# Kernel optimization log

Measured on AMD Instinct MI355X. Metric: run time of the kernel, lower is better.

The kernel has to match this reference:

```python
import jax, jax.numpy as jnp
import numpy as np

BN_EPS = 1e-5

def setup_inputs() -> dict:
    key = jax.random.key(0)
    ks = jax.random.split(key, 8)
    B, Cin, H, W = 4, 256, 64, 64
    Cqk, Cout = 128, 256
    x = jax.random.normal(ks[0], (B, Cin, H, W), dtype=jnp.float32)
    # 1x1 convs == per-pixel linear maps: weight [out, in], bias [out]
    Wq = jax.random.normal(ks[1], (Cqk, Cin), dtype=jnp.float32) * 0.05
    bq = jax.random.normal(ks[2], (Cqk,), dtype=jnp.float32) * 0.05
    Wk = jax.random.normal(ks[3], (Cqk, Cin), dtype=jnp.float32) * 0.05
    bk = jax.random.normal(ks[4], (Cqk,), dtype=jnp.float32) * 0.05
    Wv = jax.random.normal(ks[5], (Cout, Cin), dtype=jnp.float32) * 0.05
    bv = jax.random.normal(ks[6], (Cout,), dtype=jnp.float32) * 0.05
    gamma = jnp.ones((Cout,), dtype=jnp.float32)
    beta = jnp.zeros((Cout,), dtype=jnp.float32)
    return {"x": x, "Wq": Wq, "bq": bq, "Wk": Wk, "bk": bk,
            "Wv": Wv, "bv": bv, "gamma": gamma, "beta": beta}

def reference(x, Wq, bq, Wk, bk, Wv, bv, gamma, beta):
    B, Cin, H, W = x.shape
    N = H * W
    # 1x1 convs (per-pixel linear projections)
    q = jnp.einsum('bchw,oc->bohw', x, Wq) + bq[None, :, None, None]  # [B,Cqk,H,W]
    k = jnp.einsum('bchw,oc->bohw', x, Wk) + bk[None, :, None, None]  # [B,Cqk,H,W]
    v = jnp.einsum('bchw,oc->bohw', x, Wv) + bv[None, :, None, None]  # [B,Cout,H,W]
    # num_levels=1: bilinear interpolate to the same size is identity.
    qf = q.reshape(B, -1, N)   # [B,Cqk,N]
    kf = k.reshape(B, -1, N)   # [B,Cqk,N]
    vf = v.reshape(B, -1, N)   # [B,Cout,N]
    # score = q^T k, softmax over keys (no 1/sqrt(d) scaling, as in source)
    score = jnp.einsum('bcn,bcm->bnm', qf, kf)        # [B,N,N]
    att = jax.nn.softmax(score, axis=2)               # [B,N,N]
    w = jnp.einsum('bnm,bcm->bcn', att, vf)           # [B,Cout,N]
    merged = w.reshape(B, -1, H, W)                   # [B,Cout,H,W]
    # BatchNorm2d in training mode: batch stats over (B,H,W), biased variance
    mean = jnp.mean(merged, axis=(0, 2, 3), keepdims=True)
    var = jnp.var(merged, axis=(0, 2, 3), keepdims=True)
    norm = (merged - mean) * jax.lax.rsqrt(var + BN_EPS)
    return norm * gamma[None, :, None, None] + beta[None, :, None, None]
```

## Files before the change

kernel.cpp:

```cpp
#include <hip/hip_runtime.h>
#include <hip/hip_bf16.h>

typedef __attribute__((ext_vector_type(8))) _Float16 hfrag;
typedef __attribute__((ext_vector_type(4))) float ffrag;
typedef __attribute__((ext_vector_type(8))) unsigned short us8;
typedef __attribute__((ext_vector_type(4))) unsigned short us4;

#define DEVINL static __device__ __forceinline__
#define MFMAH(a, b, c)  __builtin_amdgcn_mfma_f32_16x16x32_f16((a), (b), (c), 0, 0, 0)

DEVINL void gload_lds16(const _Float16* g, _Float16* l) {
    __builtin_amdgcn_global_load_lds(
        (const __attribute__((address_space(1))) unsigned int*)g,
        (__attribute__((address_space(3))) unsigned int*)l, 16, 0, 0);
}

DEVINL int pkh(float a, float b) {
    typedef __attribute__((ext_vector_type(2))) __fp16 fp16x2;
    fp16x2 t = __builtin_amdgcn_cvt_pkrtz(a, b);
    union { fp16x2 h; int i; } u; u.h = t; return u.i;
}

DEVINL int permV(int p) {
    return (p & 35) | ((p & 8) << 1) | ((p & 4) << 1) | ((p & 16) >> 2);
}

__global__ void kprep(const float* __restrict__ Wq, const float* __restrict__ Wk,
                      const float* __restrict__ Wv, const float* __restrict__ bq,
                      const float* __restrict__ bk, const float* __restrict__ bv,
                      _Float16* __restrict__ Wh, float* __restrict__ ball) {
    int t = blockIdx.x * 256 + threadIdx.x;
    int o = t >> 8, c = t & 255;
    float v = (o < 128) ? Wq[o * 256 + c]
            : (o < 256) ? Wk[(o - 128) * 256 + c]
                        : Wv[(o - 256) * 256 + c];
    Wh[t] = (_Float16)v;
    if (c == 0) {
        ball[o] = (o < 128) ? bq[o] : (o < 256) ? bk[o - 128] : bv[o - 256];
    }
}

__global__ __launch_bounds__(256) void kproj(const float* __restrict__ x,
                                             const _Float16* __restrict__ Wh,
                                             const float* __restrict__ ball,
                                             _Float16* __restrict__ Qb,
                                             _Float16* __restrict__ Kb,
                                             _Float16* __restrict__ Vb) {
    __shared__ _Float16 sX[64 * 256];
    const int t = threadIdx.x;
    const int lane = t & 63;
    const int wv = t >> 6;
    const int l16 = lane & 15;
    const int lg = lane >> 4;
    const int b = blockIdx.x >> 6;
    const int n0 = (blockIdx.x & 63) << 6;
    const float* xb = x + (size_t)b * 256 * 4096 + n0;

    const int p = lane;
#pragma unroll
    for (int ci = 0; ci < 8; ++ci) {
        const int c0 = ci * 32 + (wv << 3);
        __align__(16) _Float16 th[8];
#pragma unroll
        for (int j = 0; j < 8; ++j) th[j] = (_Float16)xb[(size_t)(c0 + j) * 4096 + p];
        *(us8*)&sX[p * 256 + (c0 ^ ((p & 7) << 3))] = *(const us8*)th;
    }
    __syncthreads();

    ffrag accQK[16];
    ffrag accV[16];
#pragma unroll
    for (int i = 0; i < 16; ++i) {
        accQK[i] = ffrag{0.f, 0.f, 0.f, 0.f};
        accV[i]  = ffrag{0.f, 0.f, 0.f, 0.f};
    }
    const int rowx = 16 * wv + l16;
#pragma unroll
    for (int step = 0; step < 8; ++step) {
        const int cb = step * 32 + (lg << 3);
        hfrag ax = *(const hfrag*)&sX[rowx * 256 + (cb ^ ((rowx & 7) << 3))];
#pragma unroll
        for (int ct = 0; ct < 16; ++ct) {
            const int o = ct * 16 + l16;
            hfrag bw = *(const hfrag*)&Wh[o * 256 + cb];
            accQK[ct] = MFMAH(ax, bw, accQK[ct]);
        }
        hfrag bx[4];
#pragma unroll
        for (int c2 = 0; c2 < 4; ++c2) {
            const int px = c2 * 16 + l16;
            bx[c2] = *(const hfrag*)&sX[px * 256 + (cb ^ ((px & 7) << 3))];
        }
#pragma unroll
        for (int mt = 0; mt < 4; ++mt) {
            const int o = 256 + 64 * wv + 16 * mt + l16;
            hfrag aw = *(const hfrag*)&Wh[o * 256 + cb];
#pragma unroll
            for (int c2 = 0; c2 < 4; ++c2)
                accV[mt * 4 + c2] = MFMAH(aw, bx[c2], accV[mt * 4 + c2]);
        }
    }

#pragma unroll
    for (int ct = 0; ct < 16; ++ct) {
        const int o = ct * 16 + l16;
        const float bias = ball[o];
        _Float16* dst = (o < 128) ? Qb : Kb;
        const int oo = o & 127;
#pragma unroll
        for (int r = 0; r < 4; ++r) {
            const int px = 16 * wv + (lg << 2) + r;
            dst[((size_t)b * 4096 + n0 + px) * 128 + oo] = (_Float16)(accQK[ct][r] + bias);
        }
    }
#pragma unroll
    for (int mt = 0; mt < 4; ++mt) {
#pragma unroll
        for (int r = 0; r < 4; ++r) {
            const int o = 64 * wv + 16 * mt + (lg << 2) + r;
            const float bias = ball[256 + o];
#pragma unroll
            for (int c2 = 0; c2 < 4; ++c2) {
                const int px = c2 * 16 + l16;
                Vb[((size_t)b * 256 + o) * 4096 + n0 + permV(px)] =
                    (_Float16)(accV[mt * 4 + c2][r] + bias);
            }
        }
    }
}

__global__ __launch_bounds__(512, 2) void kattn(const _Float16* __restrict__ Qb,
                                                const _Float16* __restrict__ Kb,
                                                const _Float16* __restrict__ Vb,
                                                _Float16* __restrict__ pO,
                                                float* __restrict__ pML) {
    __shared__ __align__(16) _Float16 smem[49664];
    float* sml = (float*)(smem + 49152);

    const int t = threadIdx.x;
    const int lane = t & 63;
    const int wv = t >> 6;
    const int qg = wv & 3;
    const int kh = wv >> 2;
    const int l16 = lane & 15;
    const int lg = lane >> 4;

    const int blk = blockIdx.x;
    const int x8 = blk & 7;
    const int b = x8 >> 1;
    const int ksel = x8 & 1;
    const int qt5 = blk >> 3;
    const int n0 = qt5 << 7;
    const int kb = ksel << 11;

    const _Float16* Kg = Kb + (size_t)b * 4096 * 128;
    const _Float16* Vg = Vb + (size_t)b * 256 * 4096;

    hfrag aq0[4], aq1[4];
    {
        const size_t gq0 = ((size_t)b * 4096 + n0 + qg * 32 + l16) * 128;
        const size_t gq1 = gq0 + 16 * 128;
#pragma unroll
        for (int st = 0; st < 4; ++st) {
            aq0[st] = *(const hfrag*)&Qb[gq0 + st * 32 + lg * 8];
            aq1[st] = *(const hfrag*)&Qb[gq1 + st * 32 + lg * 8];
        }
    }

    float m0 = -3e38f, l0 = 0.f;
    float m1 = -3e38f, l1 = 0.f;
    ffrag O0[16], O1[16];
#pragma unroll
    for (int i = 0; i < 16; ++i) {
        O0[i] = ffrag{0.f, 0.f, 0.f, 0.f};
        O1[i] = ffrag{0.f, 0.f, 0.f, 0.f};
    }
    hfrag pb0p, pb1p;

    const int krow_in = lane >> 4;
    const int kcol = lane & 15;
    const int vrow_in = lane >> 3;
    const int vcol = lane & 7;

    auto STAGEK = [&](int it, int bsel) {
        const int k0 = kb + (it << 6);
        _Float16* sK = smem + (bsel << 13);
#pragma unroll
        for (int j = 0; j < 2; ++j) {
            const int c = 2 * wv + j;
            const int row = 4 * c + krow_in;
            gload_lds16(Kg + (size_t)(k0 + row) * 128 + ((kcol ^ (row & 7)) << 3),
                        sK + c * 512);
        }
    };
    auto STAGEV = [&](int it, int bsel) {
        const int k0 = kb + (it << 6);
        _Float16* sV = smem + 16384 + (bsel << 14);
#pragma unroll
        for (int j = 0; j < 4; ++j) {
            const int cv = 4 * wv + j;
            const int co = 8 * cv + vrow_in;
            gload_lds16(Vg + (size_t)co * 4096 + k0 + ((vcol ^ (co & 7)) << 3),
                        sV + cv * 512);
        }
    };

    auto PV = [&](int bsel) {
        const _Float16* sV = smem + 16384 + (bsel << 14);
#pragma unroll
        for (int ct = 0; ct < 16; ++ct) {
            const int co = ct * 16 + l16;
            hfrag av = *(const hfrag*)&sV[co * 64 + ((kh * 32 + lg * 8) ^ ((co & 7) << 3))];
            O0[ct] = MFMAH(av, pb0p, O0[ct]);
            O1[ct] = MFMAH(av, pb1p, O1[ct]);
        }
    };

    STAGEK(0, 0);
    STAGEV(0, 0);
    __builtin_amdgcn_sched_barrier(0);

#pragma unroll 1
    for (int it = 0; it < 32; ++it) {
        asm volatile("s_waitcnt vmcnt(4)" ::: "memory");
        __builtin_amdgcn_s_barrier();
        __builtin_amdgcn_sched_barrier(0);
        STAGEK((it + 1) & 31, (it + 1) & 1);
        __builtin_amdgcn_sched_barrier(0);

        const _Float16* sK = smem + ((it & 1) << 13);

        __builtin_amdgcn_s_setprio(1);
        ffrag S00 = ffrag{0.f,0.f,0.f,0.f}, S01 = ffrag{0.f,0.f,0.f,0.f};
        ffrag S10 = ffrag{0.f,0.f,0.f,0.f}, S11 = ffrag{0.f,0.f,0.f,0.f};
#pragma unroll
        for (int kt = 0; kt < 2; ++kt) {
            const int rowk = kh * 32 + kt * 16 + l16;
            const int swz = (rowk & 7) << 3;
#pragma unroll
            for (int st = 0; st < 4; ++st) {
                hfrag ak = *(const hfrag*)&sK[rowk * 128 + ((st * 32 + lg * 8) ^ swz)];
                if (kt == 0) {
                    S00 = MFMAH(ak, aq0[st], S00);
                    S10 = MFMAH(ak, aq1[st], S10);
                } else {
                    S01 = MFMAH(ak, aq0[st], S01);
                    S11 = MFMAH(ak, aq1[st], S11);
                }
            }
        }
        if (it > 0) PV((it - 1) & 1);
        __builtin_amdgcn_s_setprio(0);

        float mx0 = fmaxf(fmaxf(fmaxf(S00[0], S00[1]), fmaxf(S00[2], S00[3])),
                          fmaxf(fmaxf(S01[0], S01[1]), fmaxf(S01[2], S01[3])));
        float mx1 = fmaxf(fmaxf(fmaxf(S10[0], S10[1]), fmaxf(S10[2], S10[3])),
                          fmaxf(fmaxf(S11[0], S11[1]), fmaxf(S11[2], S11[3])));
        mx0 = fmaxf(mx0, __shfl_xor(mx0, 16));
        mx0 = fmaxf(mx0, __shfl_xor(mx0, 32));
        mx1 = fmaxf(mx1, __shfl_xor(mx1, 16));
        mx1 = fmaxf(mx1, __shfl_xor(mx1, 32));
        if (__any((mx0 > m0 + 8.f) || (mx1 > m1 + 8.f))) {
            const float nm0 = fmaxf(m0, mx0), nm1 = fmaxf(m1, mx1);
            const float sc0 = __expf(m0 - nm0), sc1 = __expf(m1 - nm1);
            m0 = nm0; m1 = nm1;
            l0 *= sc0; l1 *= sc1;
#pragma unroll
            for (int i = 0; i < 16; ++i) {
#pragma unroll
                for (int r = 0; r < 4; ++r) {
                    O0[i][r] *= sc0;
                    O1[i][r] *= sc1;
                }
            }
        }
        float e00[4], e01[4], e10[4], e11[4];
        float rs0 = 0.f, rs1 = 0.f;
#pragma unroll
        for (int r = 0; r < 4; ++r) {
            e00[r] = __expf(S00[r] - m0);
            e01[r] = __expf(S01[r] - m0);
            e10[r] = __expf(S10[r] - m1);
            e11[r] = __expf(S11[r] - m1);
            rs0 += e00[r] + e01[r];
            rs1 += e10[r] + e11[r];
        }
        rs0 += __shfl_xor(rs0, 16);
        rs0 += __shfl_xor(rs0, 32);
        rs1 += __shfl_xor(rs1, 16);
        rs1 += __shfl_xor(rs1, 32);
        l0 += rs0;
        l1 += rs1;

        {
            union { int i[4]; hfrag h; } u;
            u.i[0] = pkh(e00[0], e00[1]);
            u.i[1] = pkh(e00[2], e00[3]);
            u.i[2] = pkh(e01[0], e01[1]);
            u.i[3] = pkh(e01[2], e01[3]);
            pb0p = u.h;
            u.i[0] = pkh(e10[0], e10[1]);
            u.i[1] = pkh(e10[2], e10[3]);
            u.i[2] = pkh(e11[0], e11[1]);
            u.i[3] = pkh(e11[2], e11[3]);
            pb1p = u.h;
        }

        __builtin_amdgcn_s_barrier();
        __builtin_amdgcn_sched_barrier(0);
        STAGEV((it + 1) & 31, (it + 1) & 1);
        __builtin_amdgcn_sched_barrier(0);
    }

    asm volatile("s_waitcnt vmcnt(0)" ::: "memory");
    __builtin_amdgcn_s_barrier();
    PV(1);

    __syncthreads();
    _Float16* sE = smem;
    const int r0 = qg * 32 + l16;
    const int r1 = r0 + 16;
    const int rsw0 = (r0 & 7) << 3;
    const int rsw1 = (r1 & 7) << 3;
    if (kh == 1) {
        const float inv0 = 1.f / l0, inv1 = 1.f / l1;
#pragma unroll
        for (int ct = 0; ct < 16; ++ct)
#pragma unroll
            for (int r = 0; r < 4; ++r) {
                const int col = ct * 16 + lg * 4 + r;
                sE[r0 * 256 + (col ^ rsw0)] = (_Float16)(O0[ct][r] * inv0);
                sE[r1 * 256 + (col ^ rsw1)] = (_Float16)(O1[ct][r] * inv1);
            }
        if (lg == 0) {
            ((float2*)sml)[r0] = make_float2(m0, l0);
            ((float2*)sml)[r1] = make_float2(m1, l1);
        }
    }
    __syncthreads();
    const size_t mlbase = (size_t)(ksel * 4 + b) * 4096 + n0;
    if (kh == 0) {
        const float2 pml0 = ((const float2*)sml)[r0];
        const float2 pml1 = ((const float2*)sml)[r1];
        const float M0 = fmaxf(m0, pml0.x), M1 = fmaxf(m1, pml1.x);
        const float a0 = __expf(m0 - M0), c0 = __expf(pml0.x - M0);
        const float a1 = __expf(m1 - M1), c1 = __expf(pml1.x - M1);
        const float nl0 = a0 * l0 + c0 * pml0.y;
        const float nl1 = a1 * l1 + c1 * pml1.y;
        const float wa0 = a0 / nl0, wb0 = c0 * pml0.y / nl0;
        const float wa1 = a1 / nl1, wb1 = c1 * pml1.y / nl1;
        if (lg == 0) {
            ((float2*)pML)[mlbase + r0] = make_float2(M0, nl0);
            ((float2*)pML)[mlbase + r1] = make_float2(M1, nl1);
        }
#pragma unroll
        for (int ct = 0; ct < 16; ++ct)
#pragma unroll
            for (int r = 0; r < 4; ++r) {
                const int col = ct * 16 + lg * 4 + r;
                const int i0 = r0 * 256 + (col ^ rsw0);
                const int i1 = r1 * 256 + (col ^ rsw1);
                const float v0 = (float)sE[i0];
                const float v1 = (float)sE[i1];
                sE[i0] = (_Float16)(wa0 * O0[ct][r] + wb0 * v0);
                sE[i1] = (_Float16)(wa1 * O1[ct][r] + wb1 * v1);
            }
    }
    __syncthreads();
    const size_t obase = ((size_t)(ksel * 4 + b) * 4096 + n0) * 256;
#pragma unroll
    for (int i = 0; i < 8; ++i) {
        const int idx = i * 512 + t;
        const int px = idx >> 5;
        const int cg = idx & 31;
        *(us8*)&pO[obase + (size_t)px * 256 + cg * 8] =
            *(const us8*)&sE[px * 256 + (cg ^ (px & 7)) * 8];
    }
}

__global__ __launch_bounds__(256) void kmerge(const _Float16* __restrict__ pO,
                                              const float* __restrict__ pML,
                                              _Float16* __restrict__ wbuf,
                                              float* __restrict__ part) {
    __shared__ float sacc[2048];
    __shared__ float sacc2[2048];
    const int t = threadIdx.x;
    const int rowloc = t >> 5;
    const int co8 = (t & 31) * 8;
    float s[8], s2[8];
#pragma unroll
    for (int j = 0; j < 8; ++j) { s[j] = 0.f; s2[j] = 0.f; }
#pragma unroll 2
    for (int i = 0; i < 8; ++i) {
        const int g = blockIdx.x * 64 + i * 8 + rowloc;
        const float2 ml0 = ((const float2*)pML)[g];
        const float2 ml1 = ((const float2*)pML)[16384 + g];
        const float M = fmaxf(ml0.x, ml1.x);
        const float a = __expf(ml0.x - M) * ml0.y;
        const float c = __expf(ml1.x - M) * ml1.y;
        const float inv = 1.f / (a + c);
        const float wa = a * inv, wc = c * inv;
        hfrag o0 = *(const hfrag*)&pO[(size_t)g * 256 + co8];
        hfrag o1 = *(const hfrag*)&pO[(size_t)(16384 + g) * 256 + co8];
        hfrag w;
#pragma unroll
        for (int j = 0; j < 8; ++j) {
            const float v = wa * (float)o0[j] + wc * (float)o1[j];
            w[j] = (_Float16)v;
            s[j] += v;
            s2[j] += v * v;
        }
        *(hfrag*)&wbuf[(size_t)g * 256 + co8] = w;
    }
#pragma unroll
    for (int j = 0; j < 8; ++j) {
        sacc[rowloc * 256 + co8 + j] = s[j];
        sacc2[rowloc * 256 + co8 + j] = s2[j];
    }
    __syncthreads();
    float p = 0.f, p2 = 0.f;
#pragma unroll
    for (int rl = 0; rl < 8; ++rl) {
        p  += sacc[rl * 256 + t];
        p2 += sacc2[rl * 256 + t];
    }
    part[blockIdx.x * 512 + t] = p;
    part[blockIdx.x * 512 + 256 + t] = p2;
}

__global__ void kstats2(const float* __restrict__ partial, float* __restrict__ stats) {
    const int ch = blockIdx.x;
    const int j = threadIdx.x;
    float s = 0.f;
#pragma unroll
    for (int i = 0; i < 4; ++i)
        s += partial[(size_t)(j + 64 * i) * 512 + ch];
    s += __shfl_xor(s, 1);
    s += __shfl_xor(s, 2);
    s += __shfl_xor(s, 4);
    s += __shfl_xor(s, 8);
    s += __shfl_xor(s, 16);
    s += __shfl_xor(s, 32);
    if (j == 0) stats[ch] = s;
}

__global__ __launch_bounds__(256) void kapply(const _Float16* __restrict__ w,
                                              const float* __restrict__ stats,
                                              const float* __restrict__ gamma,
                                              const float* __restrict__ beta,
                                              float* __restrict__ out) {
    __shared__ _Float16 sw[64 * 260];
    __shared__ float sscale[256];
    __shared__ float sshift[256];
    const int t = threadIdx.x;
    const int b = blockIdx.x >> 6;
    const int n0 = (blockIdx.x & 63) << 6;
    const _Float16* wb = w + ((size_t)b * 4096 + n0) * 256;
#pragma unroll
    for (int i = 0; i < 16; ++i) {
        const int chunk = i * 256 + t;
        const int p = chunk >> 6;
        const int cq = chunk & 63;
        *(us4*)&sw[p * 260 + cq * 4] = *(const us4*)&wb[p * 256 + cq * 4];
    }
    {
        const float mean = stats[t] * (1.f / 16384.f);
        const float var = stats[256 + t] * (1.f / 16384.f) - mean * mean;
        const float inv = rsqrtf(var + 1e-5f);
        const float sc = gamma[t] * inv;
        sscale[t] = sc;
        sshift[t] = beta[t] - mean * sc;
    }
    __syncthreads();
    const int p = t & 63;
    const int cg = t >> 6;
    float* ob = out + (size_t)b * 256 * 4096 + n0;
#pragma unroll 4
    for (int i = 0; i < 64; ++i) {
        const int co = i * 4 + cg;
        const float v = (float)sw[p * 260 + co];
        ob[(size_t)co * 4096 + p] = v * sscale[co] + sshift[co];
    }
}

extern "C" void kernel_launch(void* const* d_in, const int* in_sizes, int n_in,
                              void* d_out, int out_size, void* d_ws, size_t ws_size,
                              hipStream_t stream) {
    const float* x     = (const float*)d_in[0];
    const float* Wq    = (const float*)d_in[1];
    const float* bq    = (const float*)d_in[2];
    const float* Wk    = (const float*)d_in[3];
    const float* bk    = (const float*)d_in[4];
    const float* Wv    = (const float*)d_in[5];
    const float* bv    = (const float*)d_in[6];
    const float* gamma = (const float*)d_in[7];
    const float* beta  = (const float*)d_in[8];
    float* out = (float*)d_out;

    char* ws = (char*)d_ws;
    _Float16* Wh    = (_Float16*)(ws + 0x0);
    float*    pML   = (float*)(ws + 0x0);
    float*    ball  = (float*)(ws + 0x40000);
    float*    stats = (float*)(ws + 0x40800);
    float*    part  = (float*)(ws + 0x41000);
    _Float16* Qb    = (_Float16*)(ws + 0x100000);
    _Float16* Kb    = (_Float16*)(ws + 0x500000);
    _Float16* wbuf  = (_Float16*)(ws + 0x100000);
    _Float16* Vb    = (_Float16*)(ws + 0x900000);
    _Float16* pO    = (_Float16*)(ws + 0x1100000);
    if (ws_size < 0x2100000) return;

    kprep<<<512, 256, 0, stream>>>(Wq, Wk, Wv, bq, bk, bv, Wh, ball);
    kproj<<<256, 256, 0, stream>>>(x, Wh, ball, Qb, Kb, Vb);
    kattn<<<256, 512, 0, stream>>>(Qb, Kb, Vb, pO, pML);
    kmerge<<<256, 256, 0, stream>>>(pO, pML, wbuf, part);
    kstats2<<<512, 64, 0, stream>>>(part, stats);
    kapply<<<256, 256, 0, stream>>>(wbuf, stats, gamma, beta, out);
}
```

Baseline: 134.8 us.

## Fuse merge, stats and BN apply into one cooperative kernel with grid sync

Replaces the kmerge, kstats2 and kapply kernels with a single cooperative kernel. Each block keeps its merged fp16 tile in shared memory, writes partial sums, and uses a grid sync before reducing stats and another before applying the normalization. This drops two kernel launches and the global round-trip of the merged buffer. In exchange it adds two grid-wide barriers and requires all 256 blocks to be co-resident.

```diff
diff --git a/kernel.cpp b/kernel.cpp
--- a/kernel.cpp
+++ b/kernel.cpp
@@ -1,5 +1,6 @@
 #include <hip/hip_runtime.h>
 #include <hip/hip_bf16.h>
+#include <hip/hip_cooperative_groups.h>
 
 typedef __attribute__((ext_vector_type(8))) _Float16 hfrag;
 typedef __attribute__((ext_vector_type(4))) float ffrag;
@@ -378,21 +379,29 @@
     }
 }
 
-__global__ __launch_bounds__(256) void kmerge(const _Float16* __restrict__ pO,
-                                              const float* __restrict__ pML,
-                                              _Float16* __restrict__ wbuf,
-                                              float* __restrict__ part) {
-    __shared__ float sacc[2048];
-    __shared__ float sacc2[2048];
+__global__ __launch_bounds__(256) void ktail(const _Float16* __restrict__ pO,
+                                             const float* __restrict__ pML,
+                                             const float* __restrict__ gamma,
+                                             const float* __restrict__ beta,
+                                             float* __restrict__ part,
+                                             float* __restrict__ stats,
+                                             float* __restrict__ out) {
+    __shared__ __align__(16) unsigned char sm[50176];
+    _Float16* sw = (_Float16*)sm;
+    float* sacc  = (float*)(sm + 33792);
+    float* sacc2 = sacc + 2048;
+
     const int t = threadIdx.x;
+    const int bid = blockIdx.x;
     const int rowloc = t >> 5;
     const int co8 = (t & 31) * 8;
+
     float s[8], s2[8];
 #pragma unroll
     for (int j = 0; j < 8; ++j) { s[j] = 0.f; s2[j] = 0.f; }
 #pragma unroll 2
     for (int i = 0; i < 8; ++i) {
-        const int g = blockIdx.x * 64 + i * 8 + rowloc;
+        const int g = bid * 64 + i * 8 + rowloc;
         const float2 ml0 = ((const float2*)pML)[g];
         const float2 ml1 = ((const float2*)pML)[16384 + g];
         const float M = fmaxf(ml0.x, ml1.x);
@@ -410,7 +419,7 @@
             s[j] += v;
             s2[j] += v * v;
         }
-        *(hfrag*)&wbuf[(size_t)g * 256 + co8] = w;
+        *(hfrag*)&sw[(i * 8 + rowloc) * 264 + co8] = w;
     }
 #pragma unroll
     for (int j = 0; j < 8; ++j) {
@@ -424,45 +433,31 @@
         p  += sacc[rl * 256 + t];
         p2 += sacc2[rl * 256 + t];
     }
-    part[blockIdx.x * 512 + t] = p;
-    part[blockIdx.x * 512 + 256 + t] = p2;
-}
-
-__global__ void kstats2(const float* __restrict__ partial, float* __restrict__ stats) {
-    const int ch = blockIdx.x;
-    const int j = threadIdx.x;
-    float s = 0.f;
-#pragma unroll
-    for (int i = 0; i < 4; ++i)
-        s += partial[(size_t)(j + 64 * i) * 512 + ch];
-    s += __shfl_xor(s, 1);
-    s += __shfl_xor(s, 2);
-    s += __shfl_xor(s, 4);
-    s += __shfl_xor(s, 8);
-    s += __shfl_xor(s, 16);
-    s += __shfl_xor(s, 32);
-    if (j == 0) stats[ch] = s;
-}
-
-__global__ __launch_bounds__(256) void kapply(const _Float16* __restrict__ w,
-                                              const float* __restrict__ stats,
-                                              const float* __restrict__ gamma,
-                                              const float* __restrict__ beta,
-                                              float* __restrict__ out) {
-    __shared__ _Float16 sw[64 * 260];
-    __shared__ float sscale[256];
-    __shared__ float sshift[256];
-    const int t = threadIdx.x;
-    const int b = blockIdx.x >> 6;
-    const int n0 = (blockIdx.x & 63) << 6;
-    const _Float16* wb = w + ((size_t)b * 4096 + n0) * 256;
-#pragma unroll
-    for (int i = 0; i < 16; ++i) {
-        const int chunk = i * 256 + t;
-        const int p = chunk >> 6;
-        const int cq = chunk & 63;
-        *(us4*)&sw[p * 260 + cq * 4] = *(const us4*)&wb[p * 256 + cq * 4];
-    }
+    part[(size_t)bid * 512 + t] = p;
+    part[(size_t)bid * 512 + 256 + t] = p2;
+
+    cooperative_groups::this_grid().sync();
+
+    {
+        const int half = t >> 7;
+        const int j = t & 127;
+        const int ch = 2 * bid + half;
+        float v = part[(size_t)j * 512 + ch] + part[(size_t)(j + 128) * 512 + ch];
+        float* red = sacc;
+        red[t] = v;
+        __syncthreads();
+#pragma unroll
+        for (int off = 64; off >= 1; off >>= 1) {
+            if ((t & 127) < off) red[t] += red[t + off];
+            __syncthreads();
+        }
+        if ((t & 127) == 0) stats[ch] = red[t];
+    }
+
+    cooperative_groups::this_grid().sync();
+
+    float* sscale = sacc;
+    float* sshift = sacc + 256;
     {
         const float mean = stats[t] * (1.f / 16384.f);
         const float var = stats[256 + t] * (1.f / 16384.f) - mean * mean;
@@ -472,14 +467,16 @@
         sshift[t] = beta[t] - mean * sc;
     }
     __syncthreads();
-    const int p = t & 63;
-    const int cg = t >> 6;
+    const int px = t & 63;
+    const int cgp = t >> 6;
+    const int b = bid >> 6;
+    const int n0 = (bid & 63) << 6;
     float* ob = out + (size_t)b * 256 * 4096 + n0;
 #pragma unroll 4
     for (int i = 0; i < 64; ++i) {
-        const int co = i * 4 + cg;
-        const float v = (float)sw[p * 260 + co];
-        ob[(size_t)co * 4096 + p] = v * sscale[co] + sshift[co];
+        const int co = i * 4 + cgp;
+        const float v = (float)sw[px * 264 + co];
+        ob[(size_t)co * 4096 + px] = v * sscale[co] + sshift[co];
     }
 }
 
@@ -505,7 +502,6 @@
     float*    part  = (float*)(ws + 0x41000);
     _Float16* Qb    = (_Float16*)(ws + 0x100000);
     _Float16* Kb    = (_Float16*)(ws + 0x500000);
-    _Float16* wbuf  = (_Float16*)(ws + 0x100000);
     _Float16* Vb    = (_Float16*)(ws + 0x900000);
     _Float16* pO    = (_Float16*)(ws + 0x1100000);
     if (ws_size < 0x2100000) return;
@@ -513,7 +509,15 @@
     kprep<<<512, 256, 0, stream>>>(Wq, Wk, Wv, bq, bk, bv, Wh, ball);
     kproj<<<256, 256, 0, stream>>>(x, Wh, ball, Qb, Kb, Vb);
     kattn<<<256, 512, 0, stream>>>(Qb, Kb, Vb, pO, pML);
-    kmerge<<<256, 256, 0, stream>>>(pO, pML, wbuf, part);
-    kstats2<<<512, 64, 0, stream>>>(part, stats);
-    kapply<<<256, 256, 0, stream>>>(wbuf, stats, gamma, beta, out);
-}
+    {
+        const _Float16* a0 = pO;
+        const float* a1 = pML;
+        const float* a2 = gamma;
+        const float* a3 = beta;
+        float* a4 = part;
+        float* a5 = stats;
+        float* a6 = out;
+        void* args[] = {&a0, &a1, &a2, &a3, &a4, &a5, &a6};
+        hipLaunchCooperativeKernel((void*)ktail, dim3(256), dim3(256), args, 0, stream);
+    }
+}
```

Result: slower. 191.3 us (+41.9%).

## Fuse split-K merge and BN stats into attention via last-block atomic counter

Applied to the files above, without the earlier changes.

The separate merge and stats-reduction kernels are removed. Each attention block now writes its partial output and increments a per-tile counter. The second-arriving block of each pair reads its partner's partial from global memory and its own from LDS, combines them, writes the merged result into pO, and atomically accumulates the per-channel sum and sum-of-squares. This cuts two kernel launches and one full round trip of the own-half partial output through global memory, at the cost of an inter-block fence/atomic handshake and float atomics, which make the statistics order nondeterministic.

```diff
diff --git a/kernel.cpp b/kernel.cpp
--- a/kernel.cpp
+++ b/kernel.cpp
@@ -28,7 +28,8 @@
 __global__ void kprep(const float* __restrict__ Wq, const float* __restrict__ Wk,
                       const float* __restrict__ Wv, const float* __restrict__ bq,
                       const float* __restrict__ bk, const float* __restrict__ bv,
-                      _Float16* __restrict__ Wh, float* __restrict__ ball) {
+                      _Float16* __restrict__ Wh, float* __restrict__ ball,
+                      int* __restrict__ cnt, float* __restrict__ stats) {
     int t = blockIdx.x * 256 + threadIdx.x;
     int o = t >> 8, c = t & 255;
     float v = (o < 128) ? Wq[o * 256 + c]
@@ -37,6 +38,11 @@
     Wh[t] = (_Float16)v;
     if (c == 0) {
         ball[o] = (o < 128) ? bq[o] : (o < 256) ? bk[o - 128] : bv[o - 256];
+    }
+    if (blockIdx.x == 0 && threadIdx.x < 128) cnt[threadIdx.x] = 0;
+    if (blockIdx.x == 1) {
+        stats[threadIdx.x] = 0.f;
+        stats[256 + threadIdx.x] = 0.f;
     }
 }
 
@@ -133,9 +139,12 @@
                                                 const _Float16* __restrict__ Kb,
                                                 const _Float16* __restrict__ Vb,
                                                 _Float16* __restrict__ pO,
-                                                float* __restrict__ pML) {
-    __shared__ __align__(16) _Float16 smem[49664];
+                                                float* __restrict__ pML,
+                                                float* __restrict__ stats,
+                                                int* __restrict__ cnt) {
+    __shared__ __align__(16) _Float16 smem[50176];
     float* sml = (float*)(smem + 49152);
+    __shared__ int sWho;
 
     const int t = threadIdx.x;
     const int lane = t & 63;
@@ -372,76 +381,76 @@
     for (int i = 0; i < 8; ++i) {
         const int idx = i * 512 + t;
         const int px = idx >> 5;
-        const int cg = idx & 31;
-        *(us8*)&pO[obase + (size_t)px * 256 + cg * 8] =
-            *(const us8*)&sE[px * 256 + (cg ^ (px & 7)) * 8];
-    }
-}
-
-__global__ __launch_bounds__(256) void kmerge(const _Float16* __restrict__ pO,
-                                              const float* __restrict__ pML,
-                                              _Float16* __restrict__ wbuf,
-                                              float* __restrict__ part) {
-    __shared__ float sacc[2048];
-    __shared__ float sacc2[2048];
-    const int t = threadIdx.x;
-    const int rowloc = t >> 5;
-    const int co8 = (t & 31) * 8;
+        const int cg8 = idx & 31;
+        *(us8*)&pO[obase + (size_t)px * 256 + cg8 * 8] =
+            *(const us8*)&sE[px * 256 + (cg8 ^ (px & 7)) * 8];
+    }
+
+    __syncthreads();
+    if (t == 0) {
+        __threadfence();
+        sWho = atomicAdd(&cnt[blk >> 1], 1);
+    }
+    __syncthreads();
+    if (sWho == 0) return;
+    if (t == 0) __threadfence();
+    __syncthreads();
+
+    float* sWab = (float*)(smem + 49664);
+    const size_t mlbaseP = (size_t)((ksel ^ 1) * 4 + b) * 4096 + n0;
+    if (t < 128) {
+        const float2 mlP = ((const float2*)pML)[mlbaseP + t];
+        const float2 mlO = ((const float2*)pML)[mlbase + t];
+        const float M = fmaxf(mlP.x, mlO.x);
+        const float a = __expf(mlP.x - M) * mlP.y;
+        const float c = __expf(mlO.x - M) * mlO.y;
+        const float inv = 1.f / (a + c);
+        ((float2*)sWab)[t] = make_float2(a * inv, c * inv);
+    }
+    __syncthreads();
+
+    const size_t gbaseP = mlbaseP * 256;
+    const size_t gbase0 = ((size_t)b * 4096 + n0) * 256;
     float s[8], s2[8];
 #pragma unroll
     for (int j = 0; j < 8; ++j) { s[j] = 0.f; s2[j] = 0.f; }
+    const int cg8 = t & 31;
 #pragma unroll 2
     for (int i = 0; i < 8; ++i) {
-        const int g = blockIdx.x * 64 + i * 8 + rowloc;
-        const float2 ml0 = ((const float2*)pML)[g];
-        const float2 ml1 = ((const float2*)pML)[16384 + g];
-        const float M = fmaxf(ml0.x, ml1.x);
-        const float a = __expf(ml0.x - M) * ml0.y;
-        const float c = __expf(ml1.x - M) * ml1.y;
-        const float inv = 1.f / (a + c);
-        const float wa = a * inv, wc = c * inv;
-        hfrag o0 = *(const hfrag*)&pO[(size_t)g * 256 + co8];
-        hfrag o1 = *(const hfrag*)&pO[(size_t)(16384 + g) * 256 + co8];
+        const int px = i * 16 + (t >> 5);
+        const float2 wab = ((const float2*)sWab)[px];
+        hfrag po = *(const hfrag*)&pO[gbaseP + (size_t)px * 256 + cg8 * 8];
+        hfrag ow = *(const hfrag*)&sE[px * 256 + (cg8 ^ (px & 7)) * 8];
         hfrag w;
 #pragma unroll
         for (int j = 0; j < 8; ++j) {
-            const float v = wa * (float)o0[j] + wc * (float)o1[j];
+            const float v = wab.x * (float)po[j] + wab.y * (float)ow[j];
             w[j] = (_Float16)v;
             s[j] += v;
             s2[j] += v * v;
         }
-        *(hfrag*)&wbuf[(size_t)g * 256 + co8] = w;
-    }
+        *(hfrag*)&pO[gbase0 + (size_t)px * 256 + cg8 * 8] = w;
+    }
+
+    __syncthreads();
+    float* sacc  = (float*)smem;
+    float* sacc2 = sacc + 4096;
+    const int rg = t >> 5;
 #pragma unroll
     for (int j = 0; j < 8; ++j) {
-        sacc[rowloc * 256 + co8 + j] = s[j];
-        sacc2[rowloc * 256 + co8 + j] = s2[j];
-    }
-    __syncthreads();
-    float p = 0.f, p2 = 0.f;
-#pragma unroll
-    for (int rl = 0; rl < 8; ++rl) {
-        p  += sacc[rl * 256 + t];
-        p2 += sacc2[rl * 256 + t];
-    }
-    part[blockIdx.x * 512 + t] = p;
-    part[blockIdx.x * 512 + 256 + t] = p2;
-}
-
-__global__ void kstats2(const float* __restrict__ partial, float* __restrict__ stats) {
-    const int ch = blockIdx.x;
-    const int j = threadIdx.x;
-    float s = 0.f;
-#pragma unroll
-    for (int i = 0; i < 4; ++i)
-        s += partial[(size_t)(j + 64 * i) * 512 + ch];
-    s += __shfl_xor(s, 1);
-    s += __shfl_xor(s, 2);
-    s += __shfl_xor(s, 4);
-    s += __shfl_xor(s, 8);
-    s += __shfl_xor(s, 16);
-    s += __shfl_xor(s, 32);
-    if (j == 0) stats[ch] = s;
+        sacc [rg * 256 + cg8 * 8 + j] = s[j];
+        sacc2[rg * 256 + cg8 * 8 + j] = s2[j];
+    }
+    __syncthreads();
+    {
+        const int ch = t & 255;
+        const int sel = t >> 8;
+        const float* src = sel ? sacc2 : sacc;
+        float sum = 0.f;
+#pragma unroll
+        for (int rg2 = 0; rg2 < 16; ++rg2) sum += src[rg2 * 256 + ch];
+        atomicAdd(&stats[sel * 256 + ch], sum);
+    }
 }
 
 __global__ __launch_bounds__(256) void kapply(const _Float16* __restrict__ w,
@@ -502,18 +511,15 @@
     float*    pML   = (float*)(ws + 0x0);
     float*    ball  = (float*)(ws + 0x40000);
     float*    stats = (float*)(ws + 0x40800);
-    float*    part  = (float*)(ws + 0x41000);
+    int*      cnt   = (int*)(ws + 0x41000);
     _Float16* Qb    = (_Float16*)(ws + 0x100000);
     _Float16* Kb    = (_Float16*)(ws + 0x500000);
-    _Float16* wbuf  = (_Float16*)(ws + 0x100000);
     _Float16* Vb    = (_Float16*)(ws + 0x900000);
     _Float16* pO    = (_Float16*)(ws + 0x1100000);
     if (ws_size < 0x2100000) return;
 
-    kprep<<<512, 256, 0, stream>>>(Wq, Wk, Wv, bq, bk, bv, Wh, ball);
+    kprep<<<512, 256, 0, stream>>>(Wq, Wk, Wv, bq, bk, bv, Wh, ball, cnt, stats);
     kproj<<<256, 256, 0, stream>>>(x, Wh, ball, Qb, Kb, Vb);
-    kattn<<<256, 512, 0, stream>>>(Qb, Kb, Vb, pO, pML);
-    kmerge<<<256, 256, 0, stream>>>(pO, pML, wbuf, part);
-    kstats2<<<512, 64, 0, stream>>>(part, stats);
-    kapply<<<256, 256, 0, stream>>>(wbuf, stats, gamma, beta, out);
-}
+    kattn<<<256, 512, 0, stream>>>(Qb, Kb, Vb, pO, pML, stats, cnt);
+    kapply<<<256, 256, 0, stream>>>(pO, stats, gamma, beta, out);
+}
```

Measured after the change: 151.8 us. +12.6%, slower.

## Replace BN stats reduction kernel with atomics and double merge/apply grid size

Applied to the files above, without the earlier changes.

Drops the separate kstats2 launch. kmerge now atomically adds per-block channel sums and sums of squares into a global stats buffer, which kprep zero-initializes. kmerge and kapply each launch 512 blocks of 32 rows instead of 256 blocks of 64, giving more parallelism on the many-CU GPU. This removes one launch and the partial-sum round trip, at the cost of global float atomic contention on 512 addresses and a nondeterministic summation order.

```diff
diff --git a/kernel.cpp b/kernel.cpp
--- a/kernel.cpp
+++ b/kernel.cpp
@@ -28,7 +28,8 @@
 __global__ void kprep(const float* __restrict__ Wq, const float* __restrict__ Wk,
                       const float* __restrict__ Wv, const float* __restrict__ bq,
                       const float* __restrict__ bk, const float* __restrict__ bv,
-                      _Float16* __restrict__ Wh, float* __restrict__ ball) {
+                      _Float16* __restrict__ Wh, float* __restrict__ ball,
+                      float* __restrict__ stats) {
     int t = blockIdx.x * 256 + threadIdx.x;
     int o = t >> 8, c = t & 255;
     float v = (o < 128) ? Wq[o * 256 + c]
@@ -37,6 +38,10 @@
     Wh[t] = (_Float16)v;
     if (c == 0) {
         ball[o] = (o < 128) ? bq[o] : (o < 256) ? bk[o - 128] : bv[o - 256];
+    }
+    if (blockIdx.x == 0) {
+        stats[threadIdx.x] = 0.f;
+        stats[256 + threadIdx.x] = 0.f;
     }
 }
 
@@ -381,9 +386,9 @@
 __global__ __launch_bounds__(256) void kmerge(const _Float16* __restrict__ pO,
                                               const float* __restrict__ pML,
                                               _Float16* __restrict__ wbuf,
-                                              float* __restrict__ part) {
-    __shared__ float sacc[2048];
-    __shared__ float sacc2[2048];
+                                              float* __restrict__ stats) {
+    __shared__ float sacc[1024];
+    __shared__ float sacc2[1024];
     const int t = threadIdx.x;
     const int rowloc = t >> 5;
     const int co8 = (t & 31) * 8;
@@ -391,8 +396,8 @@
 #pragma unroll
     for (int j = 0; j < 8; ++j) { s[j] = 0.f; s2[j] = 0.f; }
 #pragma unroll 2
-    for (int i = 0; i < 8; ++i) {
-        const int g = blockIdx.x * 64 + i * 8 + rowloc;
+    for (int i = 0; i < 4; ++i) {
+        const int g = blockIdx.x * 32 + i * 8 + rowloc;
         const float2 ml0 = ((const float2*)pML)[g];
         const float2 ml1 = ((const float2*)pML)[16384 + g];
         const float M = fmaxf(ml0.x, ml1.x);
@@ -414,34 +419,30 @@
     }
 #pragma unroll
     for (int j = 0; j < 8; ++j) {
-        sacc[rowloc * 256 + co8 + j] = s[j];
-        sacc2[rowloc * 256 + co8 + j] = s2[j];
-    }
-    __syncthreads();
-    float p = 0.f, p2 = 0.f;
-#pragma unroll
-    for (int rl = 0; rl < 8; ++rl) {
-        p  += sacc[rl * 256 + t];
-        p2 += sacc2[rl * 256 + t];
-    }
-    part[blockIdx.x * 512 + t] = p;
-    part[blockIdx.x * 512 + 256 + t] = p2;
-}
-
-__global__ void kstats2(const float* __restrict__ partial, float* __restrict__ stats) {
-    const int ch = blockIdx.x;
-    const int j = threadIdx.x;
-    float s = 0.f;
-#pragma unroll
-    for (int i = 0; i < 4; ++i)
-        s += partial[(size_t)(j + 64 * i) * 512 + ch];
-    s += __shfl_xor(s, 1);
-    s += __shfl_xor(s, 2);
-    s += __shfl_xor(s, 4);
-    s += __shfl_xor(s, 8);
-    s += __shfl_xor(s, 16);
-    s += __shfl_xor(s, 32);
-    if (j == 0) stats[ch] = s;
+        if (rowloc < 4) {
+            sacc[rowloc * 256 + co8 + j] = s[j];
+            sacc2[rowloc * 256 + co8 + j] = s2[j];
+        }
+    }
+    __syncthreads();
+    if (rowloc >= 4) {
+#pragma unroll
+        for (int j = 0; j < 8; ++j) {
+            atomicAdd(&sacc[(rowloc - 4) * 256 + co8 + j], s[j]);
+            atomicAdd(&sacc2[(rowloc - 4) * 256 + co8 + j], s2[j]);
+        }
+    }
+    __syncthreads();
+    {
+        float p = 0.f, p2 = 0.f;
+#pragma unroll
+        for (int rl = 0; rl < 4; ++rl) {
+            p  += sacc[rl * 256 + t];
+            p2 += sacc2[rl * 256 + t];
+        }
+        atomicAdd(&stats[t], p);
+        atomicAdd(&stats[256 + t], p2);
+    }
 }
 
 __global__ __launch_bounds__(256) void kapply(const _Float16* __restrict__ w,
@@ -449,15 +450,15 @@
                                               const float* __restrict__ gamma,
                                               const float* __restrict__ beta,
                                               float* __restrict__ out) {
-    __shared__ _Float16 sw[64 * 260];
+    __shared__ _Float16 sw[32 * 260];
     __shared__ float sscale[256];
     __shared__ float sshift[256];
     const int t = threadIdx.x;
-    const int b = blockIdx.x >> 6;
-    const int n0 = (blockIdx.x & 63) << 6;
+    const int b = blockIdx.x >> 7;
+    const int n0 = (blockIdx.x & 127) << 5;
     const _Float16* wb = w + ((size_t)b * 4096 + n0) * 256;
 #pragma unroll
-    for (int i = 0; i < 16; ++i) {
+    for (int i = 0; i < 8; ++i) {
         const int chunk = i * 256 + t;
         const int p = chunk >> 6;
         const int cq = chunk & 63;
@@ -472,12 +473,12 @@
         sshift[t] = beta[t] - mean * sc;
     }
     __syncthreads();
-    const int p = t & 63;
-    const int cg = t >> 6;
+    const int p = t & 31;
+    const int cg = t >> 5;
     float* ob = out + (size_t)b * 256 * 4096 + n0;
 #pragma unroll 4
-    for (int i = 0; i < 64; ++i) {
-        const int co = i * 4 + cg;
+    for (int i = 0; i < 32; ++i) {
+        const int co = i * 8 + cg;
         const float v = (float)sw[p * 260 + co];
         ob[(size_t)co * 4096 + p] = v * sscale[co] + sshift[co];
     }
@@ -502,7 +503,6 @@
     float*    pML   = (float*)(ws + 0x0);
     float*    ball  = (float*)(ws + 0x40000);
     float*    stats = (float*)(ws + 0x40800);
-    float*    part  = (float*)(ws + 0x41000);
     _Float16* Qb    = (_Float16*)(ws + 0x100000);
     _Float16* Kb    = (_Float16*)(ws + 0x500000);
     _Float16* wbuf  = (_Float16*)(ws + 0x100000);
@@ -510,10 +510,9 @@
     _Float16* pO    = (_Float16*)(ws + 0x1100000);
     if (ws_size < 0x2100000) return;
 
-    kprep<<<512, 256, 0, stream>>>(Wq, Wk, Wv, bq, bk, bv, Wh, ball);
+    kprep<<<512, 256, 0, stream>>>(Wq, Wk, Wv, bq, bk, bv, Wh, ball, stats);
     kproj<<<256, 256, 0, stream>>>(x, Wh, ball, Qb, Kb, Vb);
     kattn<<<256, 512, 0, stream>>>(Qb, Kb, Vb, pO, pML);
-    kmerge<<<256, 256, 0, stream>>>(pO, pML, wbuf, part);
-    kstats2<<<512, 64, 0, stream>>>(part, stats);
-    kapply<<<256, 256, 0, stream>>>(wbuf, stats, gamma, beta, out);
-}
+    kmerge<<<512, 256, 0, stream>>>(pO, pML, wbuf, stats);
+    kapply<<<512, 256, 0, stream>>>(wbuf, stats, gamma, beta, out);
+}
```

Result: slower. 144.0 us (+6.8%).
